# Optimization experiments

Measured on AMD Instinct MI355X. Metric: run time of the kernel, lower is better.

## Reference

```python
import jax, jax.numpy as jnp
import numpy as np

T, B, N, DIN, H = 64, 32, 64, 128, 128  # seq_len, batch, num_nodes, input_dim, hid_dim
NUM_LAYERS = 2


def _make_cell_params(key, din):
    k1, k2, k3, k4 = jax.random.split(key, 4)
    s = 0.05
    Wg = jax.random.normal(k1, (2 * (din + H), 2 * H), jnp.float32) * s  # gates (r,u)
    bg = jnp.zeros((2 * H,), jnp.float32)
    Wc = jax.random.normal(k2, (2 * (din + H), H), jnp.float32) * s      # candidate
    bc = jnp.zeros((H,), jnp.float32)
    Wq = jax.random.normal(k3, (H, H), jnp.float32) * s                  # graph learner q
    Wk = jax.random.normal(k4, (H, H), jnp.float32) * s                  # graph learner k
    return Wg, bg, Wc, bc, Wq, Wk


def setup_inputs() -> dict:
    key = jax.random.key(0)
    k_in, k_sup, k_l0, k_l1 = jax.random.split(key, 4)
    inputs = jax.random.normal(k_in, (T, B, N, DIN), jnp.float32)
    initial_hidden_state = jnp.zeros((NUM_LAYERS, B, N * H), jnp.float32)
    supports = jax.nn.softmax(jax.random.normal(k_sup, (B, N, N), jnp.float32), axis=-1)
    Wg0, bg0, Wc0, bc0, Wq0, Wk0 = _make_cell_params(k_l0, DIN)
    Wg1, bg1, Wc1, bc1, Wq1, Wk1 = _make_cell_params(k_l1, H)
    return dict(inputs=inputs, initial_hidden_state=initial_hidden_state, supports=supports,
                Wg0=Wg0, bg0=bg0, Wc0=Wc0, bc0=bc0, Wq0=Wq0, Wk0=Wk0,
                Wg1=Wg1, bg1=bg1, Wc1=Wc1, bc1=bc1, Wq1=Wq1, Wk1=Wk1)


def _cell_step(params, supports, x, h):
    # x: (B, N, din), h: (B, N, H), supports: (B, N, N)
    Wg, bg, Wc, bc, Wq, Wk = params
    xh = jnp.concatenate([x, h], axis=-1)
    conv = jnp.einsum('bnm,bmd->bnd', supports, xh)                # graph conv
    gates = jax.nn.sigmoid(jnp.concatenate([xh, conv], -1) @ Wg + bg)
    r, u = jnp.split(gates, 2, axis=-1)
    xh_r = jnp.concatenate([x, r * h], axis=-1)
    conv_c = jnp.einsum('bnm,bmd->bnd', supports, xh_r)
    c = jnp.tanh(jnp.concatenate([xh_r, conv_c], -1) @ Wc + bc)
    h_new = u * h + (1.0 - u) * c
    # dynamic graph learner: new adjacency from the updated hidden state
    scores = jnp.einsum('bnd,bmd->bnm', h_new @ Wq, h_new @ Wk)
    new_supports = jax.nn.softmax(jax.nn.relu(scores), axis=-1)
    return h_new, new_supports


def _run_layer(params, x_seq, h0, supports, din):
    # x_seq: (T, B, N*din) -> hidden sequence (T, B, N, H)
    def step(carry, x_t):
        h, sup = carry
        h_new, sup_new = _cell_step(params, sup, x_t.reshape(B, N, din), h)
        return (h_new, sup_new), h_new
    (h_last, sup_last), hs = jax.lax.scan(step, (h0.reshape(B, N, H), supports), x_seq)
    return hs, h_last, sup_last


def reference(inputs, initial_hidden_state, supports,
              Wg0, bg0, Wc0, bc0, Wq0, Wk0,
              Wg1, bg1, Wc1, bc1, Wq1, Wk1):
    layer_params = [(Wg0, bg0, Wc0, bc0, Wq0, Wk0), (Wg1, bg1, Wc1, bc1, Wq1, Wk1)]
    dins = [DIN, H]
    cur = inputs.reshape(T, B, N * DIN)
    sup = supports
    out_hidden = []
    for i in range(NUM_LAYERS):
        hs, h_last, sup = _run_layer(layer_params[i], cur, initial_hidden_state[i], sup, dins[i])
        out_hidden.append(h_last.reshape(B, N * H))
        cur = hs.reshape(T, B, N * H)
    output_hidden = jnp.stack(out_hidden, axis=0)   # (num_layers, B, N*H)
    return output_hidden, cur                        # cur: (T, B, N*H)
```

## Files before the change

kernel.cpp:

```cpp
#include <hip/hip_runtime.h>

#define TT 64
#define BB 32
#define NN 64
#define HH 128
#define NH 8192

using short8 = __attribute__((ext_vector_type(8))) short;
using f32x16 = __attribute__((ext_vector_type(16))) float;

__device__ __forceinline__ unsigned short f2bf(float f) {
  unsigned int u = __float_as_uint(f);
  u = (u + 0x7FFFu + ((u >> 16) & 1u)) >> 16;
  return (unsigned short)u;
}
__device__ __forceinline__ float bf2f(unsigned short s) {
  return __uint_as_float(((unsigned int)s) << 16);
}
__device__ __forceinline__ float sigm(float x) { return 1.0f / (1.0f + __expf(-x)); }
__device__ __forceinline__ float tanh_fast(float x) { return 2.0f / (1.0f + __expf(-2.0f * x)) - 1.0f; }

__device__ __forceinline__ uint2 pack4(float a, float b, float c, float d) {
  uint2 r;
  r.x = (unsigned int)f2bf(a) | ((unsigned int)f2bf(b) << 16);
  r.y = (unsigned int)f2bf(c) | ((unsigned int)f2bf(d) << 16);
  return r;
}
__device__ __forceinline__ short8 ldsfrag(const unsigned short* p) {
  union { uint2 u2[2]; short8 s; } f;
  f.u2[0] = *(const uint2*)p;
  f.u2[1] = *(const uint2*)(p + 4);
  return f.s;
}
__device__ __forceinline__ short8 ldgfrag(const unsigned short* p) {
  union { uint4 u4; short8 s; } f;
  f.u4 = *(const uint4*)p;
  return f.s;
}

__global__ void sglc_pack(const float* __restrict__ Wg0, const float* __restrict__ Wc0,
                          const float* __restrict__ Wq0, const float* __restrict__ Wk0,
                          const float* __restrict__ Wg1, const float* __restrict__ Wc1,
                          const float* __restrict__ Wq1, const float* __restrict__ Wk1,
                          unsigned short* __restrict__ dst) {
  int idx = blockIdx.x * 256 + threadIdx.x;
  if (idx >= 458752) return;
  int layer = idx / 229376;
  int lo = idx - layer * 229376;
  const float* src; int nkc, ncshift, off;
  if (lo < 131072)      { src = layer ? Wg1 : Wg0; nkc = 32; ncshift = 8; off = 0; }
  else if (lo < 196608) { src = layer ? Wc1 : Wc0; nkc = 32; ncshift = 7; off = 131072; }
  else if (lo < 212992) { src = layer ? Wq1 : Wq0; nkc = 8;  ncshift = 7; off = 196608; }
  else                  { src = layer ? Wk1 : Wk0; nkc = 8;  ncshift = 7; off = 212992; }
  int l2 = lo - off;
  int k = l2 >> ncshift;
  int c = l2 & ((1 << ncshift) - 1);
  int c32 = c >> 5, n32 = c & 31;
  int kc = k >> 4, kl = k & 15;
  int half = kl >> 3, j = kl & 7;
  int lane = half * 32 + n32;
  int dstoff = layer * 229376 + off + (((c32 * nkc + kc) << 9) + lane * 8 + j);
  dst[dstoff] = f2bf(src[(size_t)k * (1 << ncshift) + c]);
}

#define SX_O   0
#define SH_O   8448
#define SRH_O  16896
#define SQ_O   25344
#define SK_O   33792
#define SSUP_O 42240
#define SPT_O  46592
#define LDS_USHORTS 64000
#define SHF_BYTES 32768
#define LDS_BYTES (LDS_USHORTS * 2 + SHF_BYTES)

extern "C" __global__ void __launch_bounds__(1024, 4)
sglc_main(const float* __restrict__ Xin, const float* __restrict__ H0,
          const float* __restrict__ Sup0,
          const float* __restrict__ bg0, const float* __restrict__ bc0,
          const float* __restrict__ bg1, const float* __restrict__ bc1,
          const unsigned short* __restrict__ Wp, float* __restrict__ Out) {
  extern __shared__ unsigned short sm[];
  unsigned short* sX   = sm + SX_O;
  unsigned short* sHb  = sm + SH_O;
  unsigned short* sRH  = sm + SRH_O;
  unsigned short* sQ   = sm + SQ_O;
  unsigned short* sK   = sm + SK_O;
  unsigned short* sSup = sm + SSUP_O;
  unsigned short* sPT  = sm + SPT_O;
  float* sS  = (float*)(sm + SPT_O);
  float* uS  = (float*)(sm + SQ_O);
  float* sHf = (float*)(sm + LDS_USHORTS);

  const int b = blockIdx.x;
  const int tid = threadIdx.x;
  const int lane = tid & 63;
  const int w = tid >> 6;
  const int n32 = lane & 31;
  const int half = lane >> 5;
  const int kob = half * 8;

  float* OutH = Out;
  float* Cur  = Out + 2 * BB * NH;

  for (int layer = 0; layer < 2; ++layer) {
    const int Lw = layer * 229376;
    const float* bg = layer ? bg1 : bg0;
    const float* bc = layer ? bc1 : bc0;
    const float* xbase = layer ? Cur : Xin;
    const float* h0p = H0 + (size_t)(layer * BB + b) * NH;

    const float bgv = (w < 8) ? bg[(w & 7) * 32 + n32] : 0.0f;
    const float bcv = (w >= 4 && w < 8) ? bc[(w - 4) * 32 + n32] : 0.0f;

    {
      int r = tid >> 4, c0 = (tid & 15) * 8;
      const float* hp = h0p + r * 128 + c0;
      float4 v0 = *(const float4*)(hp);
      float4 v1 = *(const float4*)(hp + 4);
      *(uint2*)(sHb + r * 132 + c0)     = pack4(v0.x, v0.y, v0.z, v0.w);
      *(uint2*)(sHb + r * 132 + c0 + 4) = pack4(v1.x, v1.y, v1.z, v1.w);
      *(float4*)(sHf + r * 128 + c0)     = v0;
      *(float4*)(sHf + r * 128 + c0 + 4) = v1;
      const float* xp = xbase + (size_t)(0 * BB + b) * NH + r * 128 + c0;
      float4 x0 = *(const float4*)(xp);
      float4 x1 = *(const float4*)(xp + 4);
      *(uint2*)(sX + r * 132 + c0)     = pack4(x0.x, x0.y, x0.z, x0.w);
      *(uint2*)(sX + r * 132 + c0 + 4) = pack4(x1.x, x1.y, x1.z, x1.w);
      if (layer == 0) {
        int rs = tid >> 4, cs = (tid & 15) * 4;
        float4 sv = *(const float4*)(Sup0 + (size_t)b * 4096 + rs * 64 + cs);
        *(uint2*)(sSup + rs * 68 + cs) = pack4(sv.x, sv.y, sv.z, sv.w);
      }
    }
    __syncthreads();

    for (int t = 0; t < TT; ++t) {
      f32x16 acc0, acc1;
#pragma unroll
      for (int z = 0; z < 16; ++z) { acc0[z] = 0.0f; acc1[z] = 0.0f; }

      {
        const int c32g = w & 7;
        const unsigned short* wb = Wp + Lw + (((c32g * 32 + (w < 8 ? 0 : 16)) << 9) + lane * 8);
        short8 wf[4];
#pragma unroll
        for (int i = 0; i < 4; ++i) wf[i] = ldgfrag(wb + (i << 9));
#pragma unroll
        for (int kc = 0; kc < 16; ++kc) {
          short8 bf = wf[kc & 3];
          if (kc + 4 < 16) wf[kc & 3] = ldgfrag(wb + ((kc + 4) << 9));
          const unsigned short* asrc = (kc < 8) ? (sX + kc * 16 + kob) : (sHb + (kc - 8) * 16 + kob);
          short8 a0 = ldsfrag(asrc + n32 * 132);
          short8 a1 = ldsfrag(asrc + (32 + n32) * 132);
          acc0 = __builtin_amdgcn_mfma_f32_32x32x16_bf16(a0, bf, acc0, 0, 0, 0);
          acc1 = __builtin_amdgcn_mfma_f32_32x32x16_bf16(a1, bf, acc1, 0, 0, 0);
        }
        if (w >= 8) {
          unsigned short* pb = sPT + (c32g * 32 + n32) * 68;
#pragma unroll
          for (int tt = 0; tt < 2; ++tt) {
            const f32x16& ac = tt ? acc1 : acc0;
#pragma unroll
            for (int g = 0; g < 4; ++g)
              *(uint2*)(pb + tt * 32 + 8 * g + 4 * half) =
                  pack4(ac[4 * g], ac[4 * g + 1], ac[4 * g + 2], ac[4 * g + 3]);
          }
        }
      }
      __syncthreads();

      if (w < 8) {
        const int c32g = w & 7;
#pragma unroll
        for (int kc2 = 0; kc2 < 4; ++kc2) {
          short8 a0 = ldsfrag(sSup + n32 * 68 + kc2 * 16 + kob);
          short8 a1 = ldsfrag(sSup + (32 + n32) * 68 + kc2 * 16 + kob);
          short8 bf = ldsfrag(sPT + (c32g * 32 + n32) * 68 + kc2 * 16 + kob);
          acc0 = __builtin_amdgcn_mfma_f32_32x32x16_bf16(a0, bf, acc0, 0, 0, 0);
          acc1 = __builtin_amdgcn_mfma_f32_32x32x16_bf16(a1, bf, acc1, 0, 0, 0);
        }
        if (w < 4) {
          const int col = (w & 7) * 32 + n32;
#pragma unroll
          for (int tt = 0; tt < 2; ++tt) {
            const f32x16& ac = tt ? acc1 : acc0;
#pragma unroll
            for (int g = 0; g < 4; ++g)
#pragma unroll
              for (int i = 0; i < 4; ++i) {
                int row = tt * 32 + 8 * g + 4 * half + i;
                float rv = sigm(ac[4 * g + i] + bgv);
                float hv = bf2f(sHb[row * 132 + col]);
                sRH[row * 132 + col] = f2bf(rv * hv);
              }
          }
        } else {
          const int ucol = (w - 4) * 32 + n32;
#pragma unroll
          for (int tt = 0; tt < 2; ++tt) {
            const f32x16& ac = tt ? acc1 : acc0;
#pragma unroll
            for (int g = 0; g < 4; ++g)
#pragma unroll
              for (int i = 0; i < 4; ++i) {
                int row = tt * 32 + 8 * g + 4 * half + i;
                uS[row * 128 + ucol] = sigm(ac[4 * g + i] + bgv);
              }
          }
        }
      }
      __syncthreads();

      f32x16 ca0, ca1;
#pragma unroll
      for (int z = 0; z < 16; ++z) { ca0[z] = 0.0f; ca1[z] = 0.0f; }
      if (w >= 4 && w < 12) {
        const int c32c = (w < 8) ? (w - 4) : (w - 8);
        const unsigned short* wb = Wp + Lw + 131072 + (((c32c * 32 + (w < 8 ? 0 : 16)) << 9) + lane * 8);
        short8 wf[4];
#pragma unroll
        for (int i = 0; i < 4; ++i) wf[i] = ldgfrag(wb + (i << 9));
#pragma unroll
        for (int kc = 0; kc < 16; ++kc) {
          short8 bf = wf[kc & 3];
          if (kc + 4 < 16) wf[kc & 3] = ldgfrag(wb + ((kc + 4) << 9));
          const unsigned short* asrc = (kc < 8) ? (sX + kc * 16 + kob) : (sRH + (kc - 8) * 16 + kob);
          short8 a0 = ldsfrag(asrc + n32 * 132);
          short8 a1 = ldsfrag(asrc + (32 + n32) * 132);
          ca0 = __builtin_amdgcn_mfma_f32_32x32x16_bf16(a0, bf, ca0, 0, 0, 0);
          ca1 = __builtin_amdgcn_mfma_f32_32x32x16_bf16(a1, bf, ca1, 0, 0, 0);
        }
        if (w >= 8) {
          unsigned short* pb = sPT + (c32c * 32 + n32) * 68;
#pragma unroll
          for (int tt = 0; tt < 2; ++tt) {
            const f32x16& ac = tt ? ca1 : ca0;
#pragma unroll
            for (int g = 0; g < 4; ++g)
              *(uint2*)(pb + tt * 32 + 8 * g + 4 * half) =
                  pack4(ac[4 * g], ac[4 * g + 1], ac[4 * g + 2], ac[4 * g + 3]);
          }
        }
      }
      __syncthreads();

      if (w >= 4 && w < 8) {
        const int c32c = w - 4;
        const int col = c32c * 32 + n32;
#pragma unroll
        for (int kc2 = 0; kc2 < 4; ++kc2) {
          short8 a0 = ldsfrag(sSup + n32 * 68 + kc2 * 16 + kob);
          short8 a1 = ldsfrag(sSup + (32 + n32) * 68 + kc2 * 16 + kob);
          short8 bf = ldsfrag(sPT + col * 68 + kc2 * 16 + kob);
          ca0 = __builtin_amdgcn_mfma_f32_32x32x16_bf16(a0, bf, ca0, 0, 0, 0);
          ca1 = __builtin_amdgcn_mfma_f32_32x32x16_bf16(a1, bf, ca1, 0, 0, 0);
        }
        float* curp = Cur + (size_t)(t * BB + b) * NH;
#pragma unroll
        for (int tt = 0; tt < 2; ++tt) {
          const f32x16& ac = tt ? ca1 : ca0;
#pragma unroll
          for (int g = 0; g < 4; ++g)
#pragma unroll
            for (int i = 0; i < 4; ++i) {
              int row = tt * 32 + 8 * g + 4 * half + i;
              float cv = tanh_fast(ac[4 * g + i] + bcv);
              float uv = uS[row * 128 + col];
              float hold = sHf[row * 128 + col];
              float hn = uv * hold + (1.0f - uv) * cv;
              sHf[row * 128 + col] = hn;
              sHb[row * 132 + col] = f2bf(hn);
              curp[row * 128 + col] = hn;
            }
        }
      } else if (w < 4 || w >= 12) {
        if (t < TT - 1) {
          const float* xn = xbase + (size_t)((t + 1) * BB + b) * NH;
          int sidx = (w < 4 ? w : w - 8) * 64 + lane;
          int r = sidx >> 3, c0 = (sidx & 7) * 16;
          const float* sp = xn + r * 128 + c0;
          unsigned short* dp = sX + r * 132 + c0;
#pragma unroll
          for (int q4 = 0; q4 < 4; ++q4) {
            float4 v = *(const float4*)(sp + q4 * 4);
            *(uint2*)(dp + q4 * 4) = pack4(v.x, v.y, v.z, v.w);
          }
        }
      }
      __syncthreads();

      if (w >= 8) {
        const unsigned short* qb =
            Wp + Lw + ((w < 12) ? 196608 : 212992) + ((((w - 8) & 3) * 8) << 9) + lane * 8;
        const int col = ((w - 8) & 3) * 32 + n32;
        f32x16 qa0, qa1;
#pragma unroll
        for (int z = 0; z < 16; ++z) { qa0[z] = 0.0f; qa1[z] = 0.0f; }
        short8 wf[4];
#pragma unroll
        for (int i = 0; i < 4; ++i) wf[i] = ldgfrag(qb + (i << 9));
#pragma unroll
        for (int kc = 0; kc < 8; ++kc) {
          short8 bf = wf[kc & 3];
          if (kc + 4 < 8) wf[kc & 3] = ldgfrag(qb + ((kc + 4) << 9));
          short8 a0 = ldsfrag(sHb + n32 * 132 + kc * 16 + kob);
          short8 a1 = ldsfrag(sHb + (32 + n32) * 132 + kc * 16 + kob);
          qa0 = __builtin_amdgcn_mfma_f32_32x32x16_bf16(a0, bf, qa0, 0, 0, 0);
          qa1 = __builtin_amdgcn_mfma_f32_32x32x16_bf16(a1, bf, qa1, 0, 0, 0);
        }
        unsigned short* dstm = (w < 12) ? sQ : sK;
#pragma unroll
        for (int tt = 0; tt < 2; ++tt) {
          const f32x16& ac = tt ? qa1 : qa0;
#pragma unroll
          for (int g = 0; g < 4; ++g)
#pragma unroll
            for (int i = 0; i < 4; ++i)
              dstm[(tt * 32 + 8 * g + 4 * half + i) * 132 + col] = f2bf(ac[4 * g + i]);
        }
      }
      __syncthreads();

      if (w < 4) {
        const int rt = w & 1, ct = w >> 1;
        f32x16 sa;
#pragma unroll
        for (int z = 0; z < 16; ++z) sa[z] = 0.0f;
#pragma unroll
        for (int kc = 0; kc < 8; ++kc) {
          short8 a0 = ldsfrag(sQ + (rt * 32 + n32) * 132 + kc * 16 + kob);
          short8 bf = ldsfrag(sK + (ct * 32 + n32) * 132 + kc * 16 + kob);
          sa = __builtin_amdgcn_mfma_f32_32x32x16_bf16(a0, bf, sa, 0, 0, 0);
        }
#pragma unroll
        for (int g = 0; g < 4; ++g)
#pragma unroll
          for (int i = 0; i < 4; ++i)
            sS[(rt * 32 + 8 * g + 4 * half + i) * 66 + ct * 32 + n32] = fmaxf(sa[4 * g + i], 0.0f);
      }
      __syncthreads();

      {
        int row = tid >> 4, ci = (tid & 15) * 4;
        float2 v01 = *(const float2*)(sS + row * 66 + ci);
        float2 v23 = *(const float2*)(sS + row * 66 + ci + 2);
        float s0 = v01.x, s1 = v01.y, s2 = v23.x, s3 = v23.y;
        float mx = fmaxf(fmaxf(s0, s1), fmaxf(s2, s3));
#pragma unroll
        for (int off = 1; off < 16; off <<= 1) mx = fmaxf(mx, __shfl_xor(mx, off, 16));
        float e0 = __expf(s0 - mx), e1 = __expf(s1 - mx);
        float e2 = __expf(s2 - mx), e3 = __expf(s3 - mx);
        float sum = e0 + e1 + e2 + e3;
#pragma unroll
        for (int off = 1; off < 16; off <<= 1) sum += __shfl_xor(sum, off, 16);
        float inv = 1.0f / sum;
        *(uint2*)(sSup + row * 68 + ci) = pack4(e0 * inv, e1 * inv, e2 * inv, e3 * inv);
      }
      __syncthreads();
    }

    {
      float* outp = OutH + (size_t)(layer * BB + b) * NH;
      int r = tid >> 4, c0 = (tid & 15) * 8;
      *(float4*)(outp + r * 128 + c0)     = *(const float4*)(sHf + r * 128 + c0);
      *(float4*)(outp + r * 128 + c0 + 4) = *(const float4*)(sHf + r * 128 + c0 + 4);
    }
    __syncthreads();
  }
}

extern "C" void kernel_launch(void* const* d_in, const int* in_sizes, int n_in,
                              void* d_out, int out_size, void* d_ws, size_t ws_size,
                              hipStream_t stream) {
  const float* Xin  = (const float*)d_in[0];
  const float* H0   = (const float*)d_in[1];
  const float* Sup0 = (const float*)d_in[2];
  const float* Wg0  = (const float*)d_in[3];
  const float* bg0  = (const float*)d_in[4];
  const float* Wc0  = (const float*)d_in[5];
  const float* bc0  = (const float*)d_in[6];
  const float* Wq0  = (const float*)d_in[7];
  const float* Wk0  = (const float*)d_in[8];
  const float* Wg1  = (const float*)d_in[9];
  const float* bg1  = (const float*)d_in[10];
  const float* Wc1  = (const float*)d_in[11];
  const float* bc1  = (const float*)d_in[12];
  const float* Wq1  = (const float*)d_in[13];
  const float* Wk1  = (const float*)d_in[14];
  unsigned short* Wp = (unsigned short*)d_ws;

  hipFuncSetAttribute(reinterpret_cast<const void*>(sglc_main),
                      hipFuncAttributeMaxDynamicSharedMemorySize, LDS_BYTES);

  hipLaunchKernelGGL(sglc_pack, dim3(1792), dim3(256), 0, stream,
                     Wg0, Wc0, Wq0, Wk0, Wg1, Wc1, Wq1, Wk1, Wp);
  hipLaunchKernelGGL(sglc_main, dim3(BB), dim3(1024), LDS_BYTES, stream,
                     Xin, H0, Sup0, bg0, bc0, bg1, bc1, Wp, (float*)d_out);
}
```

Before: 3.039 ms.

## Overlap next-step gate x/h projection with score softmax, fuse softmax into score waves

The gate projection for step t+1 (depending only on x and the new h) now runs in the score phase of step t on waves 2-15, while waves 0-1 compute the Q·K scores and do ReLU+softmax in registers. The separate fp32 score buffer and its barrier are removed. Gate work is redistributed: waves 2-9 hold gate accumulators and waves 10-15 compute the support-side partials into sPT. This trims one barrier per step and overlaps MFMA work, at the cost of more register pressure and an uneven load across waves.

```diff
diff --git a/kernel.cpp b/kernel.cpp
--- a/kernel.cpp
+++ b/kernel.cpp
@@ -88,7 +88,6 @@
   unsigned short* sK   = sm + SK_O;
   unsigned short* sSup = sm + SSUP_O;
   unsigned short* sPT  = sm + SPT_O;
-  float* sS  = (float*)(sm + SPT_O);
   float* uS  = (float*)(sm + SQ_O);
   float* sHf = (float*)(sm + LDS_USHORTS);
 
@@ -110,7 +109,9 @@
     const float* xbase = layer ? Cur : Xin;
     const float* h0p = H0 + (size_t)(layer * BB + b) * NH;
 
-    const float bgv = (w < 8) ? bg[(w & 7) * 32 + n32] : 0.0f;
+    const bool isg = (w >= 2 && w <= 9);
+    const int gcol = (w >= 8) ? (w - 8) : w;
+    const float bgv = isg ? bg[gcol * 32 + n32] : 0.0f;
     const float bcv = (w >= 4 && w < 8) ? bc[(w - 4) * 32 + n32] : 0.0f;
 
     {
@@ -135,32 +136,51 @@
     }
     __syncthreads();
 
-    for (int t = 0; t < TT; ++t) {
-      f32x16 acc0, acc1;
-#pragma unroll
-      for (int z = 0; z < 16; ++z) { acc0[z] = 0.0f; acc1[z] = 0.0f; }
-
-      {
-        const int c32g = w & 7;
-        const unsigned short* wb = Wp + Lw + (((c32g * 32 + (w < 8 ? 0 : 16)) << 9) + lane * 8);
+    f32x16 acc0, acc1;
+
+    auto run_p1 = [&]() {
+      if (isg) {
+        const unsigned short* wb = Wp + Lw + (((gcol * 32) << 9) + lane * 8);
+#pragma unroll
+        for (int z = 0; z < 16; ++z) { acc0[z] = 0.0f; acc1[z] = 0.0f; }
         short8 wf[4];
 #pragma unroll
         for (int i = 0; i < 4; ++i) wf[i] = ldgfrag(wb + (i << 9));
 #pragma unroll
         for (int kc = 0; kc < 16; ++kc) {
-          short8 bf = wf[kc & 3];
+          short8 bfr = wf[kc & 3];
           if (kc + 4 < 16) wf[kc & 3] = ldgfrag(wb + ((kc + 4) << 9));
           const unsigned short* asrc = (kc < 8) ? (sX + kc * 16 + kob) : (sHb + (kc - 8) * 16 + kob);
           short8 a0 = ldsfrag(asrc + n32 * 132);
           short8 a1 = ldsfrag(asrc + (32 + n32) * 132);
-          acc0 = __builtin_amdgcn_mfma_f32_32x32x16_bf16(a0, bf, acc0, 0, 0, 0);
-          acc1 = __builtin_amdgcn_mfma_f32_32x32x16_bf16(a1, bf, acc1, 0, 0, 0);
-        }
-        if (w >= 8) {
+          acc0 = __builtin_amdgcn_mfma_f32_32x32x16_bf16(a0, bfr, acc0, 0, 0, 0);
+          acc1 = __builtin_amdgcn_mfma_f32_32x32x16_bf16(a1, bfr, acc1, 0, 0, 0);
+        }
+      } else if (w >= 10) {
+        const int ntile = (w < 12) ? 2 : 1;
+        for (int tt2 = 0; tt2 < ntile; ++tt2) {
+          const int c32g = (w - 10) + tt2 * 6;
+          const unsigned short* wb = Wp + Lw + (((c32g * 32 + 16) << 9) + lane * 8);
+          f32x16 pa0, pa1;
+#pragma unroll
+          for (int z = 0; z < 16; ++z) { pa0[z] = 0.0f; pa1[z] = 0.0f; }
+          short8 wf[4];
+#pragma unroll
+          for (int i = 0; i < 4; ++i) wf[i] = ldgfrag(wb + (i << 9));
+#pragma unroll
+          for (int kc = 0; kc < 16; ++kc) {
+            short8 bfr = wf[kc & 3];
+            if (kc + 4 < 16) wf[kc & 3] = ldgfrag(wb + ((kc + 4) << 9));
+            const unsigned short* asrc = (kc < 8) ? (sX + kc * 16 + kob) : (sHb + (kc - 8) * 16 + kob);
+            short8 a0 = ldsfrag(asrc + n32 * 132);
+            short8 a1 = ldsfrag(asrc + (32 + n32) * 132);
+            pa0 = __builtin_amdgcn_mfma_f32_32x32x16_bf16(a0, bfr, pa0, 0, 0, 0);
+            pa1 = __builtin_amdgcn_mfma_f32_32x32x16_bf16(a1, bfr, pa1, 0, 0, 0);
+          }
           unsigned short* pb = sPT + (c32g * 32 + n32) * 68;
 #pragma unroll
           for (int tt = 0; tt < 2; ++tt) {
-            const f32x16& ac = tt ? acc1 : acc0;
+            const f32x16& ac = tt ? pa1 : pa0;
 #pragma unroll
             for (int g = 0; g < 4; ++g)
               *(uint2*)(pb + tt * 32 + 8 * g + 4 * half) =
@@ -168,20 +188,23 @@
           }
         }
       }
-      __syncthreads();
-
-      if (w < 8) {
-        const int c32g = w & 7;
+    };
+
+    run_p1();
+    __syncthreads();
+
+    for (int t = 0; t < TT; ++t) {
+      if (isg) {
 #pragma unroll
         for (int kc2 = 0; kc2 < 4; ++kc2) {
           short8 a0 = ldsfrag(sSup + n32 * 68 + kc2 * 16 + kob);
           short8 a1 = ldsfrag(sSup + (32 + n32) * 68 + kc2 * 16 + kob);
-          short8 bf = ldsfrag(sPT + (c32g * 32 + n32) * 68 + kc2 * 16 + kob);
-          acc0 = __builtin_amdgcn_mfma_f32_32x32x16_bf16(a0, bf, acc0, 0, 0, 0);
-          acc1 = __builtin_amdgcn_mfma_f32_32x32x16_bf16(a1, bf, acc1, 0, 0, 0);
-        }
-        if (w < 4) {
-          const int col = (w & 7) * 32 + n32;
+          short8 bfr = ldsfrag(sPT + (gcol * 32 + n32) * 68 + kc2 * 16 + kob);
+          acc0 = __builtin_amdgcn_mfma_f32_32x32x16_bf16(a0, bfr, acc0, 0, 0, 0);
+          acc1 = __builtin_amdgcn_mfma_f32_32x32x16_bf16(a1, bfr, acc1, 0, 0, 0);
+        }
+        if (gcol < 4) {
+          const int col = gcol * 32 + n32;
 #pragma unroll
           for (int tt = 0; tt < 2; ++tt) {
             const f32x16& ac = tt ? acc1 : acc0;
@@ -196,7 +219,7 @@
               }
           }
         } else {
-          const int ucol = (w - 4) * 32 + n32;
+          const int ucol = (gcol - 4) * 32 + n32;
 #pragma unroll
           for (int tt = 0; tt < 2; ++tt) {
             const f32x16& ac = tt ? acc1 : acc0;
@@ -223,13 +246,13 @@
         for (int i = 0; i < 4; ++i) wf[i] = ldgfrag(wb + (i << 9));
 #pragma unroll
         for (int kc = 0; kc < 16; ++kc) {
-          short8 bf = wf[kc & 3];
+          short8 bfr = wf[kc & 3];
           if (kc + 4 < 16) wf[kc & 3] = ldgfrag(wb + ((kc + 4) << 9));
           const unsigned short* asrc = (kc < 8) ? (sX + kc * 16 + kob) : (sRH + (kc - 8) * 16 + kob);
           short8 a0 = ldsfrag(asrc + n32 * 132);
           short8 a1 = ldsfrag(asrc + (32 + n32) * 132);
-          ca0 = __builtin_amdgcn_mfma_f32_32x32x16_bf16(a0, bf, ca0, 0, 0, 0);
-          ca1 = __builtin_amdgcn_mfma_f32_32x32x16_bf16(a1, bf, ca1, 0, 0, 0);
+          ca0 = __builtin_amdgcn_mfma_f32_32x32x16_bf16(a0, bfr, ca0, 0, 0, 0);
+          ca1 = __builtin_amdgcn_mfma_f32_32x32x16_bf16(a1, bfr, ca1, 0, 0, 0);
         }
         if (w >= 8) {
           unsigned short* pb = sPT + (c32c * 32 + n32) * 68;
@@ -252,9 +275,9 @@
         for (int kc2 = 0; kc2 < 4; ++kc2) {
           short8 a0 = ldsfrag(sSup + n32 * 68 + kc2 * 16 + kob);
           short8 a1 = ldsfrag(sSup + (32 + n32) * 68 + kc2 * 16 + kob);
-          short8 bf = ldsfrag(sPT + col * 68 + kc2 * 16 + kob);
-          ca0 = __builtin_amdgcn_mfma_f32_32x32x16_bf16(a0, bf, ca0, 0, 0, 0);
-          ca1 = __builtin_amdgcn_mfma_f32_32x32x16_bf16(a1, bf, ca1, 0, 0, 0);
+          short8 bfr = ldsfrag(sPT + col * 68 + kc2 * 16 + kob);
+          ca0 = __builtin_amdgcn_mfma_f32_32x32x16_bf16(a0, bfr, ca0, 0, 0, 0);
+          ca1 = __builtin_amdgcn_mfma_f32_32x32x16_bf16(a1, bfr, ca1, 0, 0, 0);
         }
         float* curp = Cur + (size_t)(t * BB + b) * NH;
 #pragma unroll
@@ -302,12 +325,12 @@
         for (int i = 0; i < 4; ++i) wf[i] = ldgfrag(qb + (i << 9));
 #pragma unroll
         for (int kc = 0; kc < 8; ++kc) {
-          short8 bf = wf[kc & 3];
+          short8 bfr = wf[kc & 3];
           if (kc + 4 < 8) wf[kc & 3] = ldgfrag(qb + ((kc + 4) << 9));
           short8 a0 = ldsfrag(sHb + n32 * 132 + kc * 16 + kob);
           short8 a1 = ldsfrag(sHb + (32 + n32) * 132 + kc * 16 + kob);
-          qa0 = __builtin_amdgcn_mfma_f32_32x32x16_bf16(a0, bf, qa0, 0, 0, 0);
-          qa1 = __builtin_amdgcn_mfma_f32_32x32x16_bf16(a1, bf, qa1, 0, 0, 0);
+          qa0 = __builtin_amdgcn_mfma_f32_32x32x16_bf16(a0, bfr, qa0, 0, 0, 0);
+          qa1 = __builtin_amdgcn_mfma_f32_32x32x16_bf16(a1, bfr, qa1, 0, 0, 0);
         }
         unsigned short* dstm = (w < 12) ? sQ : sK;
 #pragma unroll
@@ -322,40 +345,37 @@
       }
       __syncthreads();
 
-      if (w < 4) {
-        const int rt = w & 1, ct = w >> 1;
-        f32x16 sa;
-#pragma unroll
-        for (int z = 0; z < 16; ++z) sa[z] = 0.0f;
+      if (w < 2) {
+        const int rt = w;
+        f32x16 sa0, sa1;
+#pragma unroll
+        for (int z = 0; z < 16; ++z) { sa0[z] = 0.0f; sa1[z] = 0.0f; }
 #pragma unroll
         for (int kc = 0; kc < 8; ++kc) {
           short8 a0 = ldsfrag(sQ + (rt * 32 + n32) * 132 + kc * 16 + kob);
-          short8 bf = ldsfrag(sK + (ct * 32 + n32) * 132 + kc * 16 + kob);
-          sa = __builtin_amdgcn_mfma_f32_32x32x16_bf16(a0, bf, sa, 0, 0, 0);
-        }
-#pragma unroll
-        for (int g = 0; g < 4; ++g)
-#pragma unroll
-          for (int i = 0; i < 4; ++i)
-            sS[(rt * 32 + 8 * g + 4 * half + i) * 66 + ct * 32 + n32] = fmaxf(sa[4 * g + i], 0.0f);
-      }
-      __syncthreads();
-
-      {
-        int row = tid >> 4, ci = (tid & 15) * 4;
-        float2 v01 = *(const float2*)(sS + row * 66 + ci);
-        float2 v23 = *(const float2*)(sS + row * 66 + ci + 2);
-        float s0 = v01.x, s1 = v01.y, s2 = v23.x, s3 = v23.y;
-        float mx = fmaxf(fmaxf(s0, s1), fmaxf(s2, s3));
-#pragma unroll
-        for (int off = 1; off < 16; off <<= 1) mx = fmaxf(mx, __shfl_xor(mx, off, 16));
-        float e0 = __expf(s0 - mx), e1 = __expf(s1 - mx);
-        float e2 = __expf(s2 - mx), e3 = __expf(s3 - mx);
-        float sum = e0 + e1 + e2 + e3;
-#pragma unroll
-        for (int off = 1; off < 16; off <<= 1) sum += __shfl_xor(sum, off, 16);
-        float inv = 1.0f / sum;
-        *(uint2*)(sSup + row * 68 + ci) = pack4(e0 * inv, e1 * inv, e2 * inv, e3 * inv);
+          short8 b0 = ldsfrag(sK + (n32)*132 + kc * 16 + kob);
+          short8 b1 = ldsfrag(sK + (32 + n32) * 132 + kc * 16 + kob);
+          sa0 = __builtin_amdgcn_mfma_f32_32x32x16_bf16(a0, b0, sa0, 0, 0, 0);
+          sa1 = __builtin_amdgcn_mfma_f32_32x32x16_bf16(a0, b1, sa1, 0, 0, 0);
+        }
+#pragma unroll
+        for (int j = 0; j < 16; ++j) {
+          float v0 = fmaxf(sa0[j], 0.0f);
+          float v1 = fmaxf(sa1[j], 0.0f);
+          float mx = fmaxf(v0, v1);
+#pragma unroll
+          for (int off = 1; off < 32; off <<= 1) mx = fmaxf(mx, __shfl_xor(mx, off));
+          float e0 = __expf(v0 - mx), e1 = __expf(v1 - mx);
+          float s = e0 + e1;
+#pragma unroll
+          for (int off = 1; off < 32; off <<= 1) s += __shfl_xor(s, off);
+          float inv = 1.0f / s;
+          int row = rt * 32 + (j & 3) + 8 * (j >> 2) + 4 * half;
+          sSup[row * 68 + n32]      = f2bf(e0 * inv);
+          sSup[row * 68 + 32 + n32] = f2bf(e1 * inv);
+        }
+      } else if (t < TT - 1) {
+        run_p1();
       }
       __syncthreads();
     }
```

Result: slower. 3.161 ms (+4.0%).

## Repartition per-step GEMM work across all 16 waves by row-half and column tile

Applied to the files above, without the earlier changes.

Remaps the 16 waves so each owns a 32-row half and a 32-column tile (rh, ct), instead of some waves doing both row halves while others sit idle. The gate, candidate and Q/K GEMMs are now spread over all waves, and each wave computes both the direct and propagated gate accumulators for its tile. Per-wave work in the serial recurrent phases is meant to shrink, lowering latency per timestep. The cost is duplicated weight-fragment global loads, since two waves now fetch the same B fragments.

```diff
diff --git a/kernel.cpp b/kernel.cpp
--- a/kernel.cpp
+++ b/kernel.cpp
@@ -99,6 +99,9 @@
   const int n32 = lane & 31;
   const int half = lane >> 5;
   const int kob = half * 8;
+  const int rh = w >> 3;
+  const int ct = w & 7;
+  const int arow = (rh * 32 + n32) * 132;
 
   float* OutH = Out;
   float* Cur  = Out + 2 * BB * NH;
@@ -110,8 +113,8 @@
     const float* xbase = layer ? Cur : Xin;
     const float* h0p = H0 + (size_t)(layer * BB + b) * NH;
 
-    const float bgv = (w < 8) ? bg[(w & 7) * 32 + n32] : 0.0f;
-    const float bcv = (w >= 4 && w < 8) ? bc[(w - 4) * 32 + n32] : 0.0f;
+    const float bgv = bg[ct * 32 + n32];
+    const float bcv = (ct < 4) ? bc[ct * 32 + n32] : 0.0f;
 
     {
       int r = tid >> 4, c0 = (tid & 15) * 8;
@@ -136,148 +139,124 @@
     __syncthreads();
 
     for (int t = 0; t < TT; ++t) {
-      f32x16 acc0, acc1;
-#pragma unroll
-      for (int z = 0; z < 16; ++z) { acc0[z] = 0.0f; acc1[z] = 0.0f; }
-
-      {
-        const int c32g = w & 7;
-        const unsigned short* wb = Wp + Lw + (((c32g * 32 + (w < 8 ? 0 : 16)) << 9) + lane * 8);
+      f32x16 acc;
+      f32x16 ca;
+
+      {
+        f32x16 pa;
+#pragma unroll
+        for (int z = 0; z < 16; ++z) { acc[z] = 0.0f; pa[z] = 0.0f; }
+        const unsigned short* wbd = Wp + Lw + (((ct * 32) << 9) + lane * 8);
+        const unsigned short* wbp = wbd + (16 << 9);
+        short8 wfd[4], wfp[4];
+#pragma unroll
+        for (int i = 0; i < 4; ++i) { wfd[i] = ldgfrag(wbd + (i << 9)); wfp[i] = ldgfrag(wbp + (i << 9)); }
+#pragma unroll
+        for (int kc = 0; kc < 16; ++kc) {
+          short8 bd = wfd[kc & 3], bp = wfp[kc & 3];
+          if (kc + 4 < 16) {
+            wfd[kc & 3] = ldgfrag(wbd + ((kc + 4) << 9));
+            wfp[kc & 3] = ldgfrag(wbp + ((kc + 4) << 9));
+          }
+          const unsigned short* asrc = (kc < 8) ? (sX + kc * 16 + kob) : (sHb + (kc - 8) * 16 + kob);
+          short8 a = ldsfrag(asrc + arow);
+          acc = __builtin_amdgcn_mfma_f32_32x32x16_bf16(a, bd, acc, 0, 0, 0);
+          pa  = __builtin_amdgcn_mfma_f32_32x32x16_bf16(a, bp, pa, 0, 0, 0);
+        }
+        unsigned short* pb = sPT + (ct * 32 + n32) * 68 + rh * 32;
+#pragma unroll
+        for (int g = 0; g < 4; ++g)
+          *(uint2*)(pb + 8 * g + 4 * half) =
+              pack4(pa[4 * g], pa[4 * g + 1], pa[4 * g + 2], pa[4 * g + 3]);
+      }
+      __syncthreads();
+
+      {
+#pragma unroll
+        for (int kc2 = 0; kc2 < 4; ++kc2) {
+          short8 a   = ldsfrag(sSup + (rh * 32 + n32) * 68 + kc2 * 16 + kob);
+          short8 bfr = ldsfrag(sPT + (ct * 32 + n32) * 68 + kc2 * 16 + kob);
+          acc = __builtin_amdgcn_mfma_f32_32x32x16_bf16(a, bfr, acc, 0, 0, 0);
+        }
+        if (ct < 4) {
+          const int col = ct * 32 + n32;
+#pragma unroll
+          for (int g = 0; g < 4; ++g)
+#pragma unroll
+            for (int i = 0; i < 4; ++i) {
+              int row = rh * 32 + 8 * g + 4 * half + i;
+              float rv = sigm(acc[4 * g + i] + bgv);
+              float hv = bf2f(sHb[row * 132 + col]);
+              sRH[row * 132 + col] = f2bf(rv * hv);
+            }
+        } else {
+          const int ucol = (ct - 4) * 32 + n32;
+#pragma unroll
+          for (int g = 0; g < 4; ++g)
+#pragma unroll
+            for (int i = 0; i < 4; ++i) {
+              int row = rh * 32 + 8 * g + 4 * half + i;
+              uS[row * 128 + ucol] = sigm(acc[4 * g + i] + bgv);
+            }
+        }
+      }
+      __syncthreads();
+
+      {
+#pragma unroll
+        for (int z = 0; z < 16; ++z) ca[z] = 0.0f;
+        const int isq1 = (ct < 4);
+        const int c32c = isq1 ? ct : (ct - 4);
+        const unsigned short* wb =
+            Wp + Lw + 131072 + (((c32c * 32 + (isq1 ? 0 : 16)) << 9) + lane * 8);
         short8 wf[4];
 #pragma unroll
         for (int i = 0; i < 4; ++i) wf[i] = ldgfrag(wb + (i << 9));
 #pragma unroll
         for (int kc = 0; kc < 16; ++kc) {
-          short8 bf = wf[kc & 3];
-          if (kc + 4 < 16) wf[kc & 3] = ldgfrag(wb + ((kc + 4) << 9));
-          const unsigned short* asrc = (kc < 8) ? (sX + kc * 16 + kob) : (sHb + (kc - 8) * 16 + kob);
-          short8 a0 = ldsfrag(asrc + n32 * 132);
-          short8 a1 = ldsfrag(asrc + (32 + n32) * 132);
-          acc0 = __builtin_amdgcn_mfma_f32_32x32x16_bf16(a0, bf, acc0, 0, 0, 0);
-          acc1 = __builtin_amdgcn_mfma_f32_32x32x16_bf16(a1, bf, acc1, 0, 0, 0);
-        }
-        if (w >= 8) {
-          unsigned short* pb = sPT + (c32g * 32 + n32) * 68;
-#pragma unroll
-          for (int tt = 0; tt < 2; ++tt) {
-            const f32x16& ac = tt ? acc1 : acc0;
-#pragma unroll
-            for (int g = 0; g < 4; ++g)
-              *(uint2*)(pb + tt * 32 + 8 * g + 4 * half) =
-                  pack4(ac[4 * g], ac[4 * g + 1], ac[4 * g + 2], ac[4 * g + 3]);
-          }
-        }
-      }
-      __syncthreads();
-
-      if (w < 8) {
-        const int c32g = w & 7;
-#pragma unroll
-        for (int kc2 = 0; kc2 < 4; ++kc2) {
-          short8 a0 = ldsfrag(sSup + n32 * 68 + kc2 * 16 + kob);
-          short8 a1 = ldsfrag(sSup + (32 + n32) * 68 + kc2 * 16 + kob);
-          short8 bf = ldsfrag(sPT + (c32g * 32 + n32) * 68 + kc2 * 16 + kob);
-          acc0 = __builtin_amdgcn_mfma_f32_32x32x16_bf16(a0, bf, acc0, 0, 0, 0);
-          acc1 = __builtin_amdgcn_mfma_f32_32x32x16_bf16(a1, bf, acc1, 0, 0, 0);
-        }
-        if (w < 4) {
-          const int col = (w & 7) * 32 + n32;
-#pragma unroll
-          for (int tt = 0; tt < 2; ++tt) {
-            const f32x16& ac = tt ? acc1 : acc0;
-#pragma unroll
-            for (int g = 0; g < 4; ++g)
-#pragma unroll
-              for (int i = 0; i < 4; ++i) {
-                int row = tt * 32 + 8 * g + 4 * half + i;
-                float rv = sigm(ac[4 * g + i] + bgv);
-                float hv = bf2f(sHb[row * 132 + col]);
-                sRH[row * 132 + col] = f2bf(rv * hv);
-              }
-          }
-        } else {
-          const int ucol = (w - 4) * 32 + n32;
-#pragma unroll
-          for (int tt = 0; tt < 2; ++tt) {
-            const f32x16& ac = tt ? acc1 : acc0;
-#pragma unroll
-            for (int g = 0; g < 4; ++g)
-#pragma unroll
-              for (int i = 0; i < 4; ++i) {
-                int row = tt * 32 + 8 * g + 4 * half + i;
-                uS[row * 128 + ucol] = sigm(ac[4 * g + i] + bgv);
-              }
-          }
-        }
-      }
-      __syncthreads();
-
-      f32x16 ca0, ca1;
-#pragma unroll
-      for (int z = 0; z < 16; ++z) { ca0[z] = 0.0f; ca1[z] = 0.0f; }
-      if (w >= 4 && w < 12) {
-        const int c32c = (w < 8) ? (w - 4) : (w - 8);
-        const unsigned short* wb = Wp + Lw + 131072 + (((c32c * 32 + (w < 8 ? 0 : 16)) << 9) + lane * 8);
-        short8 wf[4];
-#pragma unroll
-        for (int i = 0; i < 4; ++i) wf[i] = ldgfrag(wb + (i << 9));
-#pragma unroll
-        for (int kc = 0; kc < 16; ++kc) {
-          short8 bf = wf[kc & 3];
+          short8 bfr = wf[kc & 3];
           if (kc + 4 < 16) wf[kc & 3] = ldgfrag(wb + ((kc + 4) << 9));
           const unsigned short* asrc = (kc < 8) ? (sX + kc * 16 + kob) : (sRH + (kc - 8) * 16 + kob);
-          short8 a0 = ldsfrag(asrc + n32 * 132);
-          short8 a1 = ldsfrag(asrc + (32 + n32) * 132);
-          ca0 = __builtin_amdgcn_mfma_f32_32x32x16_bf16(a0, bf, ca0, 0, 0, 0);
-          ca1 = __builtin_amdgcn_mfma_f32_32x32x16_bf16(a1, bf, ca1, 0, 0, 0);
-        }
-        if (w >= 8) {
-          unsigned short* pb = sPT + (c32c * 32 + n32) * 68;
-#pragma unroll
-          for (int tt = 0; tt < 2; ++tt) {
-            const f32x16& ac = tt ? ca1 : ca0;
-#pragma unroll
-            for (int g = 0; g < 4; ++g)
-              *(uint2*)(pb + tt * 32 + 8 * g + 4 * half) =
-                  pack4(ac[4 * g], ac[4 * g + 1], ac[4 * g + 2], ac[4 * g + 3]);
+          short8 a = ldsfrag(asrc + arow);
+          ca = __builtin_amdgcn_mfma_f32_32x32x16_bf16(a, bfr, ca, 0, 0, 0);
+        }
+        if (!isq1) {
+          unsigned short* pb = sPT + (c32c * 32 + n32) * 68 + rh * 32;
+#pragma unroll
+          for (int g = 0; g < 4; ++g)
+            *(uint2*)(pb + 8 * g + 4 * half) =
+                pack4(ca[4 * g], ca[4 * g + 1], ca[4 * g + 2], ca[4 * g + 3]);
+        }
+      }
+      __syncthreads();
+
+      if (ct < 4) {
+        const int col = ct * 32 + n32;
+#pragma unroll
+        for (int kc2 = 0; kc2 < 4; ++kc2) {
+          short8 a   = ldsfrag(sSup + (rh * 32 + n32) * 68 + kc2 * 16 + kob);
+          short8 bfr = ldsfrag(sPT + (ct * 32 + n32) * 68 + kc2 * 16 + kob);
+          ca = __builtin_amdgcn_mfma_f32_32x32x16_bf16(a, bfr, ca, 0, 0, 0);
+        }
+        float* curp = Cur + (size_t)(t * BB + b) * NH;
+#pragma unroll
+        for (int g = 0; g < 4; ++g)
+#pragma unroll
+          for (int i = 0; i < 4; ++i) {
+            int row = rh * 32 + 8 * g + 4 * half + i;
+            float cv = tanh_fast(ca[4 * g + i] + bcv);
+            float uv = uS[row * 128 + col];
+            float hold = sHf[row * 128 + col];
+            float hn = uv * hold + (1.0f - uv) * cv;
+            sHf[row * 128 + col] = hn;
+            sHb[row * 132 + col] = f2bf(hn);
+            curp[row * 128 + col] = hn;
           }
-        }
-      }
-      __syncthreads();
-
-      if (w >= 4 && w < 8) {
-        const int c32c = w - 4;
-        const int col = c32c * 32 + n32;
-#pragma unroll
-        for (int kc2 = 0; kc2 < 4; ++kc2) {
-          short8 a0 = ldsfrag(sSup + n32 * 68 + kc2 * 16 + kob);
-          short8 a1 = ldsfrag(sSup + (32 + n32) * 68 + kc2 * 16 + kob);
-          short8 bf = ldsfrag(sPT + col * 68 + kc2 * 16 + kob);
-          ca0 = __builtin_amdgcn_mfma_f32_32x32x16_bf16(a0, bf, ca0, 0, 0, 0);
-          ca1 = __builtin_amdgcn_mfma_f32_32x32x16_bf16(a1, bf, ca1, 0, 0, 0);
-        }
-        float* curp = Cur + (size_t)(t * BB + b) * NH;
-#pragma unroll
-        for (int tt = 0; tt < 2; ++tt) {
-          const f32x16& ac = tt ? ca1 : ca0;
-#pragma unroll
-          for (int g = 0; g < 4; ++g)
-#pragma unroll
-            for (int i = 0; i < 4; ++i) {
-              int row = tt * 32 + 8 * g + 4 * half + i;
-              float cv = tanh_fast(ac[4 * g + i] + bcv);
-              float uv = uS[row * 128 + col];
-              float hold = sHf[row * 128 + col];
-              float hn = uv * hold + (1.0f - uv) * cv;
-              sHf[row * 128 + col] = hn;
-              sHb[row * 132 + col] = f2bf(hn);
-              curp[row * 128 + col] = hn;
-            }
-        }
-      } else if (w < 4 || w >= 12) {
+      } else {
         if (t < TT - 1) {
           const float* xn = xbase + (size_t)((t + 1) * BB + b) * NH;
-          int sidx = (w < 4 ? w : w - 8) * 64 + lane;
+          int sid = rh * 4 + (ct - 4);
+          int sidx = sid * 64 + lane;
           int r = sidx >> 3, c0 = (sidx & 7) * 16;
           const float* sp = xn + r * 128 + c0;
           unsigned short* dp = sX + r * 132 + c0;
@@ -290,54 +269,50 @@
       }
       __syncthreads();
 
-      if (w >= 8) {
+      {
+        const int isq = (ct < 4);
+        const int c32q = isq ? ct : (ct - 4);
         const unsigned short* qb =
-            Wp + Lw + ((w < 12) ? 196608 : 212992) + ((((w - 8) & 3) * 8) << 9) + lane * 8;
-        const int col = ((w - 8) & 3) * 32 + n32;
-        f32x16 qa0, qa1;
-#pragma unroll
-        for (int z = 0; z < 16; ++z) { qa0[z] = 0.0f; qa1[z] = 0.0f; }
+            Wp + Lw + (isq ? 196608 : 212992) + (((c32q * 8) << 9) + lane * 8);
+        f32x16 qa;
+#pragma unroll
+        for (int z = 0; z < 16; ++z) qa[z] = 0.0f;
         short8 wf[4];
 #pragma unroll
         for (int i = 0; i < 4; ++i) wf[i] = ldgfrag(qb + (i << 9));
 #pragma unroll
         for (int kc = 0; kc < 8; ++kc) {
-          short8 bf = wf[kc & 3];
+          short8 bfr = wf[kc & 3];
           if (kc + 4 < 8) wf[kc & 3] = ldgfrag(qb + ((kc + 4) << 9));
-          short8 a0 = ldsfrag(sHb + n32 * 132 + kc * 16 + kob);
-          short8 a1 = ldsfrag(sHb + (32 + n32) * 132 + kc * 16 + kob);
-          qa0 = __builtin_amdgcn_mfma_f32_32x32x16_bf16(a0, bf, qa0, 0, 0, 0);
-          qa1 = __builtin_amdgcn_mfma_f32_32x32x16_bf16(a1, bf, qa1, 0, 0, 0);
-        }
-        unsigned short* dstm = (w < 12) ? sQ : sK;
-#pragma unroll
-        for (int tt = 0; tt < 2; ++tt) {
-          const f32x16& ac = tt ? qa1 : qa0;
-#pragma unroll
-          for (int g = 0; g < 4; ++g)
-#pragma unroll
-            for (int i = 0; i < 4; ++i)
-              dstm[(tt * 32 + 8 * g + 4 * half + i) * 132 + col] = f2bf(ac[4 * g + i]);
-        }
+          short8 a = ldsfrag(sHb + arow + kc * 16 + kob);
+          qa = __builtin_amdgcn_mfma_f32_32x32x16_bf16(a, bfr, qa, 0, 0, 0);
+        }
+        unsigned short* dstm = isq ? sQ : sK;
+        const int col = c32q * 32 + n32;
+#pragma unroll
+        for (int g = 0; g < 4; ++g)
+#pragma unroll
+          for (int i = 0; i < 4; ++i)
+            dstm[(rh * 32 + 8 * g + 4 * half + i) * 132 + col] = f2bf(qa[4 * g + i]);
       }
       __syncthreads();
 
       if (w < 4) {
-        const int rt = w & 1, ct = w >> 1;
+        const int rt = w & 1, ct6 = w >> 1;
         f32x16 sa;
 #pragma unroll
         for (int z = 0; z < 16; ++z) sa[z] = 0.0f;
 #pragma unroll
         for (int kc = 0; kc < 8; ++kc) {
           short8 a0 = ldsfrag(sQ + (rt * 32 + n32) * 132 + kc * 16 + kob);
-          short8 bf = ldsfrag(sK + (ct * 32 + n32) * 132 + kc * 16 + kob);
-          sa = __builtin_amdgcn_mfma_f32_32x32x16_bf16(a0, bf, sa, 0, 0, 0);
+          short8 bfr = ldsfrag(sK + (ct6 * 32 + n32) * 132 + kc * 16 + kob);
+          sa = __builtin_amdgcn_mfma_f32_32x32x16_bf16(a0, bfr, sa, 0, 0, 0);
         }
 #pragma unroll
         for (int g = 0; g < 4; ++g)
 #pragma unroll
           for (int i = 0; i < 4; ++i)
-            sS[(rt * 32 + 8 * g + 4 * half + i) * 66 + ct * 32 + n32] = fmaxf(sa[4 * g + i], 0.0f);
+            sS[(rt * 32 + 8 * g + 4 * half + i) * 66 + ct6 * 32 + n32] = fmaxf(sa[4 * g + i], 0.0f);
       }
       __syncthreads();
 
```

Measured after the change: 3.559 ms. 17.1% more time.
